# Kernel optimization log

Measured on AMD Instinct MI355X. Metric: run time of the kernel, lower is better.

Reference implementation:

```python
import jax, jax.numpy as jnp
import numpy as np

EMB = 32  # DGM_c.input_dim

def setup_inputs() -> dict:
    key = jax.random.key(0)
    k1, k2, k3 = jax.random.split(key, 3)
    G, n, F = 32, 1024, 128
    N = G * n
    x = jax.random.normal(k1, (N, F), dtype=jnp.float32)
    W = jax.random.normal(k2, (F, EMB), dtype=jnp.float32) / np.sqrt(F)
    temperature = jnp.float32(1.0)   # nn.Parameter init 1.0
    threshold = jnp.float32(0.5)     # nn.Parameter init 0.5
    batch = jnp.repeat(jnp.arange(G, dtype=jnp.int32), n)  # equal-sized graphs
    edge_index = jax.random.randint(k3, (2, 262144), 0, N, dtype=jnp.int32)
    return {"x": x, "W": W, "temperature": temperature, "threshold": threshold,
            "batch": batch, "edge_index": edge_index, "num_graphs": G}


def reference(x, W, temperature, threshold, batch, edge_index, num_graphs):
    # x: [N, F]; equal-sized graphs of n nodes each (batch is sorted, contiguous)
    N = x.shape[0]
    G = num_graphs
    n = N // G

    # embed_f: linear projection to EMB dims (edge structure unused by this embed_f)
    xe = x @ W                                  # [N, EMB]

    # scale<0 branch fires only for the FIRST graph; centroid/scale are detached
    x0 = xe[:n]                                 # graph 0 embedding
    centroid = jax.lax.stop_gradient(jnp.mean(x0, axis=0))             # [EMB]
    scale = jax.lax.stop_gradient(0.9 / jnp.max(jnp.abs(x0 - centroid)))

    xg = ((xe - centroid) * scale).reshape(G, n, EMB)

    # squared pairwise euclidean distances per graph (cdist**2, clamped >= 0)
    sq = jnp.sum(xg * xg, axis=-1)              # [G, n]
    D = jnp.maximum(sq[:, :, None] + sq[:, None, :]
                    - 2.0 * jnp.einsum('gnd,gmd->gnm', xg, xg), 0.0)   # [G, n, n]

    A = jax.nn.sigmoid(temperature * (jnp.abs(threshold) - D))         # [G, n, n]

    # sigmoid > 0 everywhere => dense_to_sparse keeps every entry, row-major,
    # with per-graph node offsets added back.
    edge_weight = A.reshape(-1)                 # [G*n*n]
    ii = jnp.arange(n, dtype=jnp.int32)
    gi = jnp.broadcast_to(ii[:, None], (n, n)).reshape(-1)  # row index
    gj = jnp.broadcast_to(ii[None, :], (n, n)).reshape(-1)  # col index
    off = (jnp.arange(G, dtype=jnp.int32) * n)[:, None]     # [G, 1]
    src = (off + gi[None, :]).reshape(-1)
    dst = (off + gj[None, :]).reshape(-1)
    edge_index_out = jnp.stack([src, dst])      # [2, G*n*n]

    return xe, edge_index_out, edge_weight
```

## Files before the change

kernel.cpp:

```cpp
#include <hip/hip_runtime.h>

#define FDIM 128
#define EMB 32

typedef __attribute__((ext_vector_type(4))) float f32x4;

static __device__ __forceinline__ void store_nt(float* p, float4 v) {
    f32x4 w; w.x = v.x; w.y = v.y; w.z = v.z; w.w = v.w;
    __builtin_nontemporal_store(w, (f32x4*)p);
}

__global__ __launch_bounds__(256) void k_gemm(const float* __restrict__ x,
                                              const float* __restrict__ Wm,
                                              float* __restrict__ xe) {
    __shared__ float sW[FDIM * EMB];
    const int t = threadIdx.x;
#pragma unroll
    for (int i = 0; i < (FDIM * EMB) / (256 * 4); ++i) {
        int idx = (t + i * 256) * 4;
        *(float4*)(sW + idx) = *(const float4*)(Wm + idx);
    }
    __syncthreads();

    const int r0 = blockIdx.x * 128 + (t >> 3) * 4;
    const int e0 = (t & 7) * 4;

    float acc[4][4];
#pragma unroll
    for (int i = 0; i < 4; ++i)
#pragma unroll
        for (int j = 0; j < 4; ++j) acc[i][j] = 0.f;

    for (int k = 0; k < FDIM; k += 4) {
        float4 w0 = *(const float4*)(sW + (k + 0) * EMB + e0);
        float4 w1 = *(const float4*)(sW + (k + 1) * EMB + e0);
        float4 w2 = *(const float4*)(sW + (k + 2) * EMB + e0);
        float4 w3 = *(const float4*)(sW + (k + 3) * EMB + e0);
#pragma unroll
        for (int rr = 0; rr < 4; ++rr) {
            float4 xq = *(const float4*)(x + (size_t)(r0 + rr) * FDIM + k);
            acc[rr][0] += xq.x * w0.x + xq.y * w1.x + xq.z * w2.x + xq.w * w3.x;
            acc[rr][1] += xq.x * w0.y + xq.y * w1.y + xq.z * w2.y + xq.w * w3.y;
            acc[rr][2] += xq.x * w0.z + xq.y * w1.z + xq.z * w2.z + xq.w * w3.z;
            acc[rr][3] += xq.x * w0.w + xq.y * w1.w + xq.z * w2.w + xq.w * w3.w;
        }
    }

#pragma unroll
    for (int rr = 0; rr < 4; ++rr) {
        const size_t r = (size_t)(r0 + rr);
        float4 o; o.x = acc[rr][0]; o.y = acc[rr][1]; o.z = acc[rr][2]; o.w = acc[rr][3];
        *(float4*)(xe + r * EMB + e0) = o;
    }
}

__global__ __launch_bounds__(256) void k_stats_a(const float* __restrict__ xe,
                                                 float* __restrict__ psum,
                                                 float* __restrict__ pmin,
                                                 float* __restrict__ pmax) {
    __shared__ float rs[256], rmn[256], rmx[256];
    const int t = threadIdx.x;
    const int d = t & 31, rg = t >> 5;
    const int r0 = blockIdx.x * 32;

    float s = 0.f, mn = 3.4e38f, mx = -3.4e38f;
#pragma unroll
    for (int it = 0; it < 4; ++it) {
        float v = xe[(size_t)(r0 + rg + it * 8) * EMB + d];
        s += v; mn = fminf(mn, v); mx = fmaxf(mx, v);
    }
    rs[t] = s; rmn[t] = mn; rmx[t] = mx;
    __syncthreads();
#pragma unroll
    for (int st = 128; st >= 32; st >>= 1) {
        if (t < st) {
            rs[t] += rs[t + st];
            rmn[t] = fminf(rmn[t], rmn[t + st]);
            rmx[t] = fmaxf(rmx[t], rmx[t + st]);
        }
        __syncthreads();
    }
    if (t < 32) {
        psum[blockIdx.x * 32 + t] = rs[t];
        pmin[blockIdx.x * 32 + t] = rmn[t];
        pmax[blockIdx.x * 32 + t] = rmx[t];
    }
}

__global__ __launch_bounds__(64) void k_stats_b(const float* __restrict__ psum,
                                                const float* __restrict__ pmin,
                                                const float* __restrict__ pmax,
                                                int nb, int n,
                                                float* __restrict__ stats) {
    const int t = threadIdx.x;
    const int d = t & 31;
    float s = 0.f, mn = 3.4e38f, mx = -3.4e38f;
    for (int b = 0; b < nb; ++b) {
        s += psum[b * 32 + d];
        mn = fminf(mn, pmin[b * 32 + d]);
        mx = fmaxf(mx, pmax[b * 32 + d]);
    }
    const float c = s / (float)n;
    float dev = fmaxf(mx - c, c - mn);
#pragma unroll
    for (int off = 16; off >= 1; off >>= 1)
        dev = fmaxf(dev, __shfl_xor(dev, off, 32));
    if (t < 32) stats[t] = c;
    if (t == 0) stats[EMB] = 0.9f / dev;
}

#define LDST 36
__global__ __launch_bounds__(256) void k_edges(const float* __restrict__ xe,
                                               const float* __restrict__ stats,
                                               const float* __restrict__ tptr,
                                               const float* __restrict__ thptr,
                                               float* __restrict__ wts,
                                               float* __restrict__ srcp,
                                               float* __restrict__ dstp,
                                               int n) {
    __shared__ float shA[64 * LDST];
    __shared__ float shB[64 * LDST];
    __shared__ float sqA[64], sqB[64];

    const int g = blockIdx.z;
    const int i0 = blockIdx.y * 64, j0 = blockIdx.x * 64;
    const int t = threadIdx.x;
    const float scale = stats[EMB];

    const float* baseA = xe + ((size_t)g * n + i0) * EMB;
    const float* baseB = xe + ((size_t)g * n + j0) * EMB;

#pragma unroll
    for (int c = 0; c < 2; ++c) {
        int id = t + c * 256;
        int row = id >> 3;
        int dc = (id & 7) * 4;
        int dswz = dc ^ (((row >> 2) & 7) << 2);
        float4 cen = *(const float4*)(stats + dc);
        float4 va = *(const float4*)(baseA + (size_t)row * EMB + dc);
        float4 vb = *(const float4*)(baseB + (size_t)row * EMB + dc);
        va.x = (va.x - cen.x) * scale; va.y = (va.y - cen.y) * scale;
        va.z = (va.z - cen.z) * scale; va.w = (va.w - cen.w) * scale;
        vb.x = (vb.x - cen.x) * scale; vb.y = (vb.y - cen.y) * scale;
        vb.z = (vb.z - cen.z) * scale; vb.w = (vb.w - cen.w) * scale;
        *(float4*)(shA + row * LDST + dc) = va;
        *(float4*)(shB + row * LDST + dswz) = vb;
    }
    __syncthreads();

    if (t < 64) {
        float s = 0.f;
#pragma unroll
        for (int d = 0; d < EMB; d += 4) {
            float4 v = *(const float4*)(shA + t * LDST + d);
            s += v.x * v.x + v.y * v.y + v.z * v.z + v.w * v.w;
        }
        sqA[t] = s;
    } else if (t < 128) {
        int r = t - 64;
        int key = ((r >> 2) & 7) << 2;
        float s = 0.f;
#pragma unroll
        for (int d = 0; d < EMB; d += 4) {
            float4 v = *(const float4*)(shB + r * LDST + (d ^ key));
            s += v.x * v.x + v.y * v.y + v.z * v.z + v.w * v.w;
        }
        sqB[r] = s;
    }
    __syncthreads();

    const int ti = t >> 4, tj = t & 15;
    const int bkey = (tj & 7) << 2;
    float acc[4][4];
#pragma unroll
    for (int i = 0; i < 4; ++i)
#pragma unroll
        for (int j = 0; j < 4; ++j) acc[i][j] = 0.f;

    for (int d = 0; d < EMB; d += 4) {
        float4 a[4], b[4];
#pragma unroll
        for (int u = 0; u < 4; ++u)
            a[u] = *(const float4*)(shA + (ti * 4 + u) * LDST + d);
        const int dsw = d ^ bkey;
#pragma unroll
        for (int v = 0; v < 4; ++v)
            b[v] = *(const float4*)(shB + (tj * 4 + v) * LDST + dsw);
#pragma unroll
        for (int u = 0; u < 4; ++u)
#pragma unroll
            for (int v = 0; v < 4; ++v)
                acc[u][v] += a[u].x * b[v].x + a[u].y * b[v].y +
                             a[u].z * b[v].z + a[u].w * b[v].w;
    }

    const float T = *tptr;
    const float TH = fabsf(*thptr);
    const int gn = g * n;
    const size_t gbase = (size_t)g * n * n;

    const float4 sq4 = *(const float4*)(sqB + tj * 4);
    const float dbase = (float)(gn + j0 + tj * 4);
    float4 dst4; dst4.x = dbase; dst4.y = dbase + 1.f; dst4.z = dbase + 2.f; dst4.w = dbase + 3.f;

#pragma unroll
    for (int u = 0; u < 4; ++u) {
        const int row = i0 + ti * 4 + u;
        const float sa = sqA[ti * 4 + u];
        const size_t off = gbase + (size_t)row * n + j0 + tj * 4;

        float4 w;
        {
            float D0 = fmaxf(sa + sq4.x - 2.f * acc[u][0], 0.f);
            float D1 = fmaxf(sa + sq4.y - 2.f * acc[u][1], 0.f);
            float D2 = fmaxf(sa + sq4.z - 2.f * acc[u][2], 0.f);
            float D3 = fmaxf(sa + sq4.w - 2.f * acc[u][3], 0.f);
            w.x = __builtin_amdgcn_rcpf(1.f + __expf(-(T * (TH - D0))));
            w.y = __builtin_amdgcn_rcpf(1.f + __expf(-(T * (TH - D1))));
            w.z = __builtin_amdgcn_rcpf(1.f + __expf(-(T * (TH - D2))));
            w.w = __builtin_amdgcn_rcpf(1.f + __expf(-(T * (TH - D3))));
        }
        store_nt(wts + off, w);

        const float sv = (float)(gn + row);
        float4 s4; s4.x = sv; s4.y = sv; s4.z = sv; s4.w = sv;
        store_nt(srcp + off, s4);
        store_nt(dstp + off, dst4);
    }
}

extern "C" void kernel_launch(void* const* d_in, const int* in_sizes, int n_in,
                              void* d_out, int out_size, void* d_ws, size_t ws_size,
                              hipStream_t stream) {
    const float* x     = (const float*)d_in[0];
    const float* Wm    = (const float*)d_in[1];
    const float* tptr  = (const float*)d_in[2];
    const float* thptr = (const float*)d_in[3];

    const int N = in_sizes[0] / FDIM;
    const long long rem = (long long)out_size - (long long)N * EMB;
    int G = (rem > 0) ? (int)((3LL * N * N) / rem) : 32;
    if (G <= 0) G = 32;
    const int n = N / G;
    const int nb = n / 32;

    float* out  = (float*)d_out;
    float* xe   = out;
    const long long M = (long long)G * n * n;
    float* srcp = out + (size_t)N * EMB;
    float* dstp = srcp + (size_t)M;
    float* wts  = dstp + (size_t)M;

    float* stats = (float*)d_ws;
    float* psum  = stats + 64;
    float* pmin  = psum + (size_t)nb * 32;
    float* pmax  = pmin + (size_t)nb * 32;

    k_gemm<<<N / 128, 256, 0, stream>>>(x, Wm, xe);
    k_stats_a<<<nb, 256, 0, stream>>>(xe, psum, pmin, pmax);
    k_stats_b<<<1, 64, 0, stream>>>(psum, pmin, pmax, nb, n, stats);
    dim3 ge(n / 64, n / 64, G);
    k_edges<<<ge, 256, 0, stream>>>(xe, stats, tptr, thptr, wts, srcp, dstp, n);
}
```

Measured before the change: 99.89 us.

## Enlarge edge tile to 128x128 with 8x8 register blocking and swizzled LDS

The edge kernel now computes 128x128 output tiles per block, with each thread holding an 8x8 accumulator, instead of 64x64 tiles with 4x4 per thread. Both A and B tiles use an XOR-swizzled unpadded LDS layout. Squared norms are computed during the load using shuffles, which removes one barrier and a separate pass. The aim is fewer blocks and more reuse per LDS load, at the cost of higher register pressure. The kernel is dominated by output writes, so the gain is likely limited.

```diff
diff --git a/kernel.cpp b/kernel.cpp
--- a/kernel.cpp
+++ b/kernel.cpp
@@ -109,7 +109,7 @@
     if (t == 0) stats[EMB] = 0.9f / dev;
 }
 
-#define LDST 36
+#define KEY(r) (((((r) >> 2) & 7) ^ (((r) >> 5) & 1)) << 2)
 __global__ __launch_bounds__(256) void k_edges(const float* __restrict__ xe,
                                                const float* __restrict__ stats,
                                                const float* __restrict__ tptr,
@@ -118,80 +118,77 @@
                                                float* __restrict__ srcp,
                                                float* __restrict__ dstp,
                                                int n) {
-    __shared__ float shA[64 * LDST];
-    __shared__ float shB[64 * LDST];
-    __shared__ float sqA[64], sqB[64];
+    __shared__ float shA[128 * 32];
+    __shared__ float shB[128 * 32];
+    __shared__ float sqA[128], sqB[128];
 
     const int g = blockIdx.z;
-    const int i0 = blockIdx.y * 64, j0 = blockIdx.x * 64;
+    const int i0 = blockIdx.y * 128, j0 = blockIdx.x * 128;
     const int t = threadIdx.x;
     const float scale = stats[EMB];
 
-    const float* baseA = xe + ((size_t)g * n + i0) * EMB;
-    const float* baseB = xe + ((size_t)g * n + j0) * EMB;
-
-#pragma unroll
-    for (int c = 0; c < 2; ++c) {
+#pragma unroll
+    for (int c = 0; c < 8; ++c) {
         int id = t + c * 256;
-        int row = id >> 3;
+        int side = id >> 10;
+        int row = (id >> 3) & 127;
         int dc = (id & 7) * 4;
-        int dswz = dc ^ (((row >> 2) & 7) << 2);
+        int dswz = dc ^ KEY(row);
+        int grow = (side ? j0 : i0) + row;
         float4 cen = *(const float4*)(stats + dc);
-        float4 va = *(const float4*)(baseA + (size_t)row * EMB + dc);
-        float4 vb = *(const float4*)(baseB + (size_t)row * EMB + dc);
-        va.x = (va.x - cen.x) * scale; va.y = (va.y - cen.y) * scale;
-        va.z = (va.z - cen.z) * scale; va.w = (va.w - cen.w) * scale;
-        vb.x = (vb.x - cen.x) * scale; vb.y = (vb.y - cen.y) * scale;
-        vb.z = (vb.z - cen.z) * scale; vb.w = (vb.w - cen.w) * scale;
-        *(float4*)(shA + row * LDST + dc) = va;
-        *(float4*)(shB + row * LDST + dswz) = vb;
+        float4 v = *(const float4*)(xe + ((size_t)g * n + grow) * EMB + dc);
+        v.x = (v.x - cen.x) * scale; v.y = (v.y - cen.y) * scale;
+        v.z = (v.z - cen.z) * scale; v.w = (v.w - cen.w) * scale;
+        float* sh = side ? shB : shA;
+        *(float4*)(sh + row * 32 + dswz) = v;
+        float ps = v.x * v.x + v.y * v.y + v.z * v.z + v.w * v.w;
+        ps += __shfl_xor(ps, 1);
+        ps += __shfl_xor(ps, 2);
+        ps += __shfl_xor(ps, 4);
+        if ((t & 7) == 0) { if (side) sqB[row] = ps; else sqA[row] = ps; }
     }
     __syncthreads();
 
-    if (t < 64) {
-        float s = 0.f;
-#pragma unroll
-        for (int d = 0; d < EMB; d += 4) {
-            float4 v = *(const float4*)(shA + t * LDST + d);
-            s += v.x * v.x + v.y * v.y + v.z * v.z + v.w * v.w;
-        }
-        sqA[t] = s;
-    } else if (t < 128) {
-        int r = t - 64;
-        int key = ((r >> 2) & 7) << 2;
-        float s = 0.f;
-#pragma unroll
-        for (int d = 0; d < EMB; d += 4) {
-            float4 v = *(const float4*)(shB + r * LDST + (d ^ key));
-            s += v.x * v.x + v.y * v.y + v.z * v.z + v.w * v.w;
-        }
-        sqB[r] = s;
-    }
-    __syncthreads();
-
-    const int ti = t >> 4, tj = t & 15;
-    const int bkey = (tj & 7) << 2;
-    float acc[4][4];
-#pragma unroll
-    for (int i = 0; i < 4; ++i)
-#pragma unroll
-        for (int j = 0; j < 4; ++j) acc[i][j] = 0.f;
-
+    const int ty = t >> 4, tx = t & 15;
+    int rowA[8], ka[8];
+#pragma unroll
+    for (int u = 0; u < 8; ++u) {
+        int r = ty * 8 + u;
+        rowA[u] = r * 32;
+        ka[u] = KEY(r);
+    }
+    int rowB[4], kb[4];
+#pragma unroll
+    for (int v = 0; v < 4; ++v) {
+        int r = tx * 4 + v;
+        rowB[v] = r * 32;
+        kb[v] = KEY(r);
+    }
+
+    float acc[8][8];
+#pragma unroll
+    for (int i = 0; i < 8; ++i)
+#pragma unroll
+        for (int j = 0; j < 8; ++j) acc[i][j] = 0.f;
+
+#pragma unroll
     for (int d = 0; d < EMB; d += 4) {
-        float4 a[4], b[4];
-#pragma unroll
-        for (int u = 0; u < 4; ++u)
-            a[u] = *(const float4*)(shA + (ti * 4 + u) * LDST + d);
-        const int dsw = d ^ bkey;
-#pragma unroll
-        for (int v = 0; v < 4; ++v)
-            b[v] = *(const float4*)(shB + (tj * 4 + v) * LDST + dsw);
-#pragma unroll
-        for (int u = 0; u < 4; ++u)
-#pragma unroll
-            for (int v = 0; v < 4; ++v)
-                acc[u][v] += a[u].x * b[v].x + a[u].y * b[v].y +
-                             a[u].z * b[v].z + a[u].w * b[v].w;
+        float4 a[8];
+#pragma unroll
+        for (int u = 0; u < 8; ++u)
+            a[u] = *(const float4*)(shA + rowA[u] + (d ^ ka[u]));
+#pragma unroll
+        for (int v = 0; v < 4; ++v) {
+            const int ds = d ^ kb[v];
+            float4 b = *(const float4*)(shB + rowB[v] + ds);
+#pragma unroll
+            for (int u = 0; u < 8; ++u)
+                acc[u][v] += a[u].x * b.x + a[u].y * b.y + a[u].z * b.z + a[u].w * b.w;
+            float4 b2 = *(const float4*)(shB + rowB[v] + 64 * 32 + ds);
+#pragma unroll
+            for (int u = 0; u < 8; ++u)
+                acc[u][v + 4] += a[u].x * b2.x + a[u].y * b2.y + a[u].z * b2.z + a[u].w * b2.w;
+        }
     }
 
     const float T = *tptr;
@@ -199,33 +196,47 @@
     const int gn = g * n;
     const size_t gbase = (size_t)g * n * n;
 
-    const float4 sq4 = *(const float4*)(sqB + tj * 4);
-    const float dbase = (float)(gn + j0 + tj * 4);
-    float4 dst4; dst4.x = dbase; dst4.y = dbase + 1.f; dst4.z = dbase + 2.f; dst4.w = dbase + 3.f;
-
-#pragma unroll
-    for (int u = 0; u < 4; ++u) {
-        const int row = i0 + ti * 4 + u;
-        const float sa = sqA[ti * 4 + u];
-        const size_t off = gbase + (size_t)row * n + j0 + tj * 4;
-
-        float4 w;
+    const float4 sq1 = *(const float4*)(sqB + tx * 4);
+    const float4 sq2 = *(const float4*)(sqB + 64 + tx * 4);
+    const float db1 = (float)(gn + j0 + tx * 4);
+    const float db2 = db1 + 64.f;
+    float4 dstA; dstA.x = db1; dstA.y = db1 + 1.f; dstA.z = db1 + 2.f; dstA.w = db1 + 3.f;
+    float4 dstB; dstB.x = db2; dstB.y = db2 + 1.f; dstB.z = db2 + 2.f; dstB.w = db2 + 3.f;
+
+#pragma unroll
+    for (int u = 0; u < 8; ++u) {
+        const int row = i0 + ty * 8 + u;
+        const float sa = sqA[ty * 8 + u];
+        const size_t off = gbase + (size_t)row * n + j0 + tx * 4;
+
+        float4 w1, w2;
         {
-            float D0 = fmaxf(sa + sq4.x - 2.f * acc[u][0], 0.f);
-            float D1 = fmaxf(sa + sq4.y - 2.f * acc[u][1], 0.f);
-            float D2 = fmaxf(sa + sq4.z - 2.f * acc[u][2], 0.f);
-            float D3 = fmaxf(sa + sq4.w - 2.f * acc[u][3], 0.f);
-            w.x = __builtin_amdgcn_rcpf(1.f + __expf(-(T * (TH - D0))));
-            w.y = __builtin_amdgcn_rcpf(1.f + __expf(-(T * (TH - D1))));
-            w.z = __builtin_amdgcn_rcpf(1.f + __expf(-(T * (TH - D2))));
-            w.w = __builtin_amdgcn_rcpf(1.f + __expf(-(T * (TH - D3))));
-        }
-        store_nt(wts + off, w);
+            float D0 = fmaxf(sa + sq1.x - 2.f * acc[u][0], 0.f);
+            float D1 = fmaxf(sa + sq1.y - 2.f * acc[u][1], 0.f);
+            float D2 = fmaxf(sa + sq1.z - 2.f * acc[u][2], 0.f);
+            float D3 = fmaxf(sa + sq1.w - 2.f * acc[u][3], 0.f);
+            w1.x = __builtin_amdgcn_rcpf(1.f + __expf(-(T * (TH - D0))));
+            w1.y = __builtin_amdgcn_rcpf(1.f + __expf(-(T * (TH - D1))));
+            w1.z = __builtin_amdgcn_rcpf(1.f + __expf(-(T * (TH - D2))));
+            w1.w = __builtin_amdgcn_rcpf(1.f + __expf(-(T * (TH - D3))));
+            float E0 = fmaxf(sa + sq2.x - 2.f * acc[u][4], 0.f);
+            float E1 = fmaxf(sa + sq2.y - 2.f * acc[u][5], 0.f);
+            float E2 = fmaxf(sa + sq2.z - 2.f * acc[u][6], 0.f);
+            float E3 = fmaxf(sa + sq2.w - 2.f * acc[u][7], 0.f);
+            w2.x = __builtin_amdgcn_rcpf(1.f + __expf(-(T * (TH - E0))));
+            w2.y = __builtin_amdgcn_rcpf(1.f + __expf(-(T * (TH - E1))));
+            w2.z = __builtin_amdgcn_rcpf(1.f + __expf(-(T * (TH - E2))));
+            w2.w = __builtin_amdgcn_rcpf(1.f + __expf(-(T * (TH - E3))));
+        }
+        store_nt(wts + off, w1);
+        store_nt(wts + off + 64, w2);
 
         const float sv = (float)(gn + row);
         float4 s4; s4.x = sv; s4.y = sv; s4.z = sv; s4.w = sv;
         store_nt(srcp + off, s4);
-        store_nt(dstp + off, dst4);
+        store_nt(srcp + off + 64, s4);
+        store_nt(dstp + off, dstA);
+        store_nt(dstp + off + 64, dstB);
     }
 }
 
@@ -259,6 +270,6 @@
     k_gemm<<<N / 128, 256, 0, stream>>>(x, Wm, xe);
     k_stats_a<<<nb, 256, 0, stream>>>(xe, psum, pmin, pmax);
     k_stats_b<<<1, 64, 0, stream>>>(psum, pmin, pmax, nb, n, stats);
-    dim3 ge(n / 64, n / 64, G);
+    dim3 ge(n / 128, n / 128, G);
     k_edges<<<ge, 256, 0, stream>>>(xe, stats, tptr, thptr, wts, srcp, dstp, n);
 }
```

Result: slower. 145.2 us (+45.4%).

## Use packed fp16 dot2 for pairwise Gram tile with transposed LDS layout

Applied to the files above, without the earlier changes.

The edge kernel now converts the centred and scaled embeddings to packed fp16 pairs and stores them in a transposed dimension-major shared layout. The inner product uses the fdot2 instruction, halving LDS traffic and FMA count. Squared norms are computed in fp32 during the load via shuffles, which removes a separate pass and one barrier. This lowers precision of the distance cross term, which may perturb sigmoid weights. The kernel is likely bound by writing the large output arrays, so the compute savings may matter little.

```diff
diff --git a/kernel.cpp b/kernel.cpp
--- a/kernel.cpp
+++ b/kernel.cpp
@@ -4,10 +4,25 @@
 #define EMB 32
 
 typedef __attribute__((ext_vector_type(4))) float f32x4;
+typedef __fp16 h2 __attribute__((ext_vector_type(2)));
 
 static __device__ __forceinline__ void store_nt(float* p, float4 v) {
     f32x4 w; w.x = v.x; w.y = v.y; w.z = v.z; w.w = v.w;
     __builtin_nontemporal_store(w, (f32x4*)p);
+}
+
+static __device__ __forceinline__ unsigned pkh2(float x, float y) {
+    h2 h = __builtin_amdgcn_cvt_pkrtz(x, y);
+    union { h2 h; unsigned u; } c; c.h = h; return c.u;
+}
+
+static __device__ __forceinline__ float fdot2u(unsigned a, unsigned b, float c) {
+    union { unsigned u; h2 h; } ua, ub; ua.u = a; ub.u = b;
+#if __has_builtin(__builtin_amdgcn_fdot2)
+    return __builtin_amdgcn_fdot2(ua.h, ub.h, c, false);
+#else
+    return c + (float)ua.h.x * (float)ub.h.x + (float)ua.h.y * (float)ub.h.y;
+#endif
 }
 
 __global__ __launch_bounds__(256) void k_gemm(const float* __restrict__ x,
@@ -109,7 +124,7 @@
     if (t == 0) stats[EMB] = 0.9f / dev;
 }
 
-#define LDST 36
+#define DPS 68
 __global__ __launch_bounds__(256) void k_edges(const float* __restrict__ xe,
                                                const float* __restrict__ stats,
                                                const float* __restrict__ tptr,
@@ -118,9 +133,10 @@
                                                float* __restrict__ srcp,
                                                float* __restrict__ dstp,
                                                int n) {
-    __shared__ float shA[64 * LDST];
-    __shared__ float shB[64 * LDST];
-    __shared__ float sqA[64], sqB[64];
+    __shared__ unsigned shA[16 * DPS];
+    __shared__ unsigned shB[16 * DPS];
+    __shared__ __attribute__((aligned(16))) float sqA[64];
+    __shared__ __attribute__((aligned(16))) float sqB[64];
 
     const int g = blockIdx.z;
     const int i0 = blockIdx.y * 64, j0 = blockIdx.x * 64;
@@ -135,7 +151,7 @@
         int id = t + c * 256;
         int row = id >> 3;
         int dc = (id & 7) * 4;
-        int dswz = dc ^ (((row >> 2) & 7) << 2);
+        int dp = dc >> 1;
         float4 cen = *(const float4*)(stats + dc);
         float4 va = *(const float4*)(baseA + (size_t)row * EMB + dc);
         float4 vb = *(const float4*)(baseB + (size_t)row * EMB + dc);
@@ -143,55 +159,37 @@
         va.z = (va.z - cen.z) * scale; va.w = (va.w - cen.w) * scale;
         vb.x = (vb.x - cen.x) * scale; vb.y = (vb.y - cen.y) * scale;
         vb.z = (vb.z - cen.z) * scale; vb.w = (vb.w - cen.w) * scale;
-        *(float4*)(shA + row * LDST + dc) = va;
-        *(float4*)(shB + row * LDST + dswz) = vb;
+        shA[dp * DPS + row]       = pkh2(va.x, va.y);
+        shA[(dp + 1) * DPS + row] = pkh2(va.z, va.w);
+        shB[dp * DPS + row]       = pkh2(vb.x, vb.y);
+        shB[(dp + 1) * DPS + row] = pkh2(vb.z, vb.w);
+        float pa = va.x * va.x + va.y * va.y + va.z * va.z + va.w * va.w;
+        float pb = vb.x * vb.x + vb.y * vb.y + vb.z * vb.z + vb.w * vb.w;
+        pa += __shfl_xor(pa, 1); pb += __shfl_xor(pb, 1);
+        pa += __shfl_xor(pa, 2); pb += __shfl_xor(pb, 2);
+        pa += __shfl_xor(pa, 4); pb += __shfl_xor(pb, 4);
+        if ((t & 7) == 0) { sqA[row] = pa; sqB[row] = pb; }
     }
     __syncthreads();
 
-    if (t < 64) {
-        float s = 0.f;
-#pragma unroll
-        for (int d = 0; d < EMB; d += 4) {
-            float4 v = *(const float4*)(shA + t * LDST + d);
-            s += v.x * v.x + v.y * v.y + v.z * v.z + v.w * v.w;
-        }
-        sqA[t] = s;
-    } else if (t < 128) {
-        int r = t - 64;
-        int key = ((r >> 2) & 7) << 2;
-        float s = 0.f;
-#pragma unroll
-        for (int d = 0; d < EMB; d += 4) {
-            float4 v = *(const float4*)(shB + r * LDST + (d ^ key));
-            s += v.x * v.x + v.y * v.y + v.z * v.z + v.w * v.w;
-        }
-        sqB[r] = s;
-    }
-    __syncthreads();
-
     const int ti = t >> 4, tj = t & 15;
-    const int bkey = (tj & 7) << 2;
     float acc[4][4];
 #pragma unroll
     for (int i = 0; i < 4; ++i)
 #pragma unroll
         for (int j = 0; j < 4; ++j) acc[i][j] = 0.f;
 
-    for (int d = 0; d < EMB; d += 4) {
-        float4 a[4], b[4];
+#pragma unroll
+    for (int dp = 0; dp < 16; ++dp) {
+        uint4 ua = *(const uint4*)(shA + dp * DPS + ti * 4);
+        uint4 ub = *(const uint4*)(shB + dp * DPS + tj * 4);
+        unsigned av[4] = { ua.x, ua.y, ua.z, ua.w };
+        unsigned bv[4] = { ub.x, ub.y, ub.z, ub.w };
 #pragma unroll
         for (int u = 0; u < 4; ++u)
-            a[u] = *(const float4*)(shA + (ti * 4 + u) * LDST + d);
-        const int dsw = d ^ bkey;
-#pragma unroll
-        for (int v = 0; v < 4; ++v)
-            b[v] = *(const float4*)(shB + (tj * 4 + v) * LDST + dsw);
-#pragma unroll
-        for (int u = 0; u < 4; ++u)
 #pragma unroll
             for (int v = 0; v < 4; ++v)
-                acc[u][v] += a[u].x * b[v].x + a[u].y * b[v].y +
-                             a[u].z * b[v].z + a[u].w * b[v].w;
+                acc[u][v] = fdot2u(av[u], bv[v], acc[u][v]);
     }
 
     const float T = *tptr;
```

Result: slower. 108.3 us (+8.4%).
